# Kernel optimization log

Measured on AMD Instinct MI355X. Metric: run time of the kernel, lower is better.

## Reference

```python
import jax, jax.numpy as jnp
import numpy as np
import math

B, L, D = 8, 2048, 256
NUM_TYPES = 1
T_MAX = 200.0
SIGMA = 1.0


def setup_inputs() -> dict:
    key = jax.random.key(0)
    ks = jax.random.split(key, 12)
    event_type = jnp.ones((B, L), dtype=jnp.int64 if jax.config.jax_enable_x64 else jnp.int32)
    t = jax.random.uniform(ks[0], (B, L), dtype=jnp.float32) * T_MAX
    event_time = jnp.sort(t, axis=-1)
    s = 1.0 / math.sqrt(D)
    emb_weight = jax.random.normal(ks[1], (NUM_TYPES + 1, D), jnp.float32)
    emb_weight = emb_weight.at[0].set(0.0)  # padding_idx=0
    gate_w = jax.random.normal(ks[2], (2, D), jnp.float32) * s
    gate_b = jnp.zeros((2,), jnp.float32)
    ker_w = jax.random.normal(ks[3], (1, D), jnp.float32) * s
    ker_b = jnp.zeros((1,), jnp.float32)
    ln_gamma = jnp.ones((D,), jnp.float32)
    ln_beta = jnp.zeros((D,), jnp.float32)
    gen_input_w = jax.random.normal(ks[4], (D, D), jnp.float32) * s
    gen_noise_w = jax.random.normal(ks[5], (D, D), jnp.float32) * s
    gen_out_w = jax.random.normal(ks[6], (1, D), jnp.float32) * s
    gen_out_b = jnp.zeros((1,), jnp.float32)
    noise = jax.random.uniform(ks[7], (B, L, D), jnp.float32)  # torch.rand noise in Generator
    return dict(event_type=event_type, event_time=event_time, emb_weight=emb_weight,
                gate_w=gate_w, gate_b=gate_b, ker_w=ker_w, ker_b=ker_b,
                ln_gamma=ln_gamma, ln_beta=ln_beta, gen_input_w=gen_input_w,
                gen_noise_w=gen_noise_w, gen_out_w=gen_out_w, gen_out_b=gen_out_b,
                noise=noise)


def _softplus_beta(x, beta):
    return jax.nn.softplus(beta * x) / beta


def reference(event_type, event_time, emb_weight, gate_w, gate_b, ker_w, ker_b,
              ln_gamma, ln_beta, gen_input_w, gen_noise_w, gen_out_w, gen_out_b, noise):
    d_model = emb_weight.shape[-1]
    # ---- temporal positional encoding (this is `embedding`) ----
    pos_vec = jnp.power(10000.0, 2.0 * jnp.arange(d_model, dtype=jnp.float32) / d_model)
    t = event_time[:, :, None] / pos_vec                      # [B,L,D]
    idx = jnp.arange(d_model)
    temp_enc = jnp.where(idx % 2 == 0, jnp.sin(t), jnp.cos(t))
    # ---- type embedding ----
    te = emb_weight[event_type] * math.sqrt(d_model)          # [B,L,D]
    # ---- pairwise |t_i - t_j| ; xt[b,i,j]=t_i, xt_bar[b,i,j]=t_j ----
    dt = jnp.abs(event_time[:, :, None] - event_time[:, None, :])  # [B,L,L]
    # ---- squared exponential kernel: params depend only on row i (xd[b,i,j]=te[b,i]) ----
    ls = _softplus_beta(te @ ker_w.T + ker_b, 0.2)[..., 0]    # [B,L]
    scores_k = (SIGMA ** 2) * jnp.exp(-(dt ** 2) / (ls[:, :, None] ** 2))
    # ---- sigmoid gate ----
    p = jax.nn.sigmoid(te @ gate_w.T + gate_b)                # [B,L,2]
    l = p[..., 0][:, :, None]
    s = p[..., 1][:, :, None]
    gate = 1.0 + 0.5 * jnp.tanh((dt / T_MAX - l) / s)
    scores = scores_k * gate                                  # [B,L,L]
    # ---- causal mask: strictly-upper-triangle -> -1e10, then softmax ----
    causal = jnp.tril(jnp.ones((event_time.shape[1], event_time.shape[1]), jnp.bool_))
    scores = jnp.where(causal[None], scores, -1e10)
    attn = jax.nn.softmax(scores, axis=-1)
    # ---- hidden = attn @ temp_enc, layernorm ----
    hidden = jnp.einsum('bij,bjd->bid', attn, temp_enc)
    mu = hidden.mean(-1, keepdims=True)
    var = hidden.var(-1, keepdims=True)
    hidden = (hidden - mu) / jnp.sqrt(var + 1e-6) * ln_gamma + ln_beta
    # ---- Generator (dropout in eval = identity) ----
    h = jax.nn.relu(noise @ gen_noise_w.T + hidden @ gen_input_w.T)
    out = jax.nn.softplus(h @ gen_out_w.T + gen_out_b)[..., 0]  # [B,L]
    return out
```

## Files before the change

kernel.cpp:

```cpp
#include <hip/hip_runtime.h>
#include <hip/hip_bf16.h>

#define BD 8
#define LD 2048
#define DD 256
#define LOG2E 1.4426950408889634f

typedef unsigned short ushort_t;
typedef __attribute__((ext_vector_type(8))) short short8;
typedef __attribute__((ext_vector_type(4))) float floatx4;

__device__ __forceinline__ ushort_t f2bfu(float x) {
  __hip_bfloat16 h = __float2bfloat16(x);
  return *reinterpret_cast<ushort_t*>(&h);
}

__device__ __forceinline__ float exp2fast(float x) {
#if __has_builtin(__builtin_amdgcn_exp2f)
  return __builtin_amdgcn_exp2f(x);
#else
  return __expf(x * 0.6931471805599453f);
#endif
}

__device__ __forceinline__ void dma16(const ushort_t* g, ushort_t* l) {
  __builtin_amdgcn_global_load_lds(
      (const __attribute__((address_space(1))) unsigned int*)g,
      (__attribute__((address_space(3))) unsigned int*)l,
      16, 0, 0);
}

__device__ __forceinline__ float sin_acc(float a) {
  float k = rintf(a * 0.15915494f);
  float r = __builtin_fmaf(-k, 6.2831855f, a);
  r = __builtin_fmaf(-k, -1.7484555e-7f, r);
  return __sinf(r);
}
__device__ __forceinline__ float cos_acc(float a) {
  float k = rintf(a * 0.15915494f);
  float r = __builtin_fmaf(-k, 6.2831855f, a);
  r = __builtin_fmaf(-k, -1.7484555e-7f, r);
  return __cosf(r);
}

__device__ __forceinline__ short8 pk8(float4 a, float4 b) {
  short8 r;
  r[0] = (short)f2bfu(a.x); r[1] = (short)f2bfu(a.y);
  r[2] = (short)f2bfu(a.z); r[3] = (short)f2bfu(a.w);
  r[4] = (short)f2bfu(b.x); r[5] = (short)f2bfu(b.y);
  r[6] = (short)f2bfu(b.z); r[7] = (short)f2bfu(b.w);
  return r;
}

__global__ __launch_bounds__(256) void k_prep(
    const float* __restrict__ etime, const float* __restrict__ embw,
    const float* __restrict__ gatew, const float* __restrict__ gateb,
    const float* __restrict__ kerw, const float* __restrict__ kerb,
    const float* __restrict__ wn, const float* __restrict__ wi,
    ushort_t* __restrict__ enc_bf, ushort_t* __restrict__ wcat,
    float* __restrict__ ptable)
{
  const int bk = blockIdx.x;
  const int tid = threadIdx.x;
  __shared__ float ts[32];
  __shared__ float red[4][3];
  if (bk < 512) {
    if (tid < 32) ts[tid] = etime[(bk >> 6) * LD + (bk & 63) * 32 + tid];
    __syncthreads();
    uint4* dst = (uint4*)(enc_bf + (size_t)bk * 8192);
    #pragma unroll
    for (int jblk = 0; jblk < 4; ++jblk) {
      const int idx4 = jblk * 256 + tid;
      const int d = ((idx4 >> 6) << 4) | (idx4 & 15);
      const int jb = ((idx4 >> 4) & 3) * 8;
      float freq = __expf(-0.07195578416f * (float)d);
      unsigned int pk[4];
      #pragma unroll
      for (int p = 0; p < 4; ++p) {
        float a0 = ts[jb + 2 * p] * freq;
        float a1 = ts[jb + 2 * p + 1] * freq;
        float v0 = (d & 1) ? cos_acc(a0) : sin_acc(a0);
        float v1 = (d & 1) ? cos_acc(a1) : sin_acc(a1);
        pk[p] = (unsigned int)f2bfu(v0) | ((unsigned int)f2bfu(v1) << 16);
      }
      dst[idx4] = make_uint4(pk[0], pk[1], pk[2], pk[3]);
    }
  } else if (bk < 640) {
    int p = (bk - 512) * 256 + tid;
    int c = p >> 7;
    int k = (p & 127) * 4;
    const float* src = (k < 256) ? (wn + c * 256 + k) : (wi + c * 256 + (k - 256));
    float4 f = *(const float4*)src;
    ushort4 u;
    u.x = f2bfu(f.x); u.y = f2bfu(f.y); u.z = f2bfu(f.z); u.w = f2bfu(f.w);
    *(ushort4*)(wcat + (size_t)c * 512 + k) = u;
  } else {
    int d = tid;
    int lane = d & 63, wvi = d >> 6;
    for (int ty = 0; ty < 2; ++ty) {
      float te = embw[ty * DD + d] * 16.0f;
      float p1 = te * kerw[d];
      float p2 = te * gatew[d];
      float p3 = te * gatew[DD + d];
      #pragma unroll
      for (int off = 32; off > 0; off >>= 1) {
        p1 += __shfl_xor(p1, off);
        p2 += __shfl_xor(p2, off);
        p3 += __shfl_xor(p3, off);
      }
      if (lane == 0) { red[wvi][0] = p1; red[wvi][1] = p2; red[wvi][2] = p3; }
      __syncthreads();
      if (d == 0) {
        float s1 = red[0][0] + red[1][0] + red[2][0] + red[3][0] + kerb[0];
        float s2 = red[0][1] + red[1][1] + red[2][1] + red[3][1] + gateb[0];
        float s3 = red[0][2] + red[1][2] + red[2][2] + red[3][2] + gateb[1];
        float z = 0.2f * s1;
        float sp = (z > 15.0f) ? z : log1pf(__expf(z));
        float ls = 5.0f * sp;
        float il = 1.0f / (ls * ls);
        float l  = 1.0f / (1.0f + __expf(-s2));
        float s  = 1.0f / (1.0f + __expf(-s3));
        float is2 = 2.0f / s;
        ptable[ty * 4 + 0] = -il * LOG2E;
        ptable[ty * 4 + 1] = 0.005f * is2 * LOG2E;
        ptable[ty * 4 + 2] = l * is2 * LOG2E;
      }
      __syncthreads();
    }
  }
}

__global__ __launch_bounds__(512, 2) void k_attn(
    const ushort_t* __restrict__ enc_bf, const float* __restrict__ etime,
    const int* __restrict__ etype, const float* __restrict__ ptable,
    const float* __restrict__ gamma, const float* __restrict__ beta,
    ushort_t* __restrict__ hidden_bf)
{
  __shared__ __align__(16) ushort_t stage[8][8192];
  const int tid = threadIdx.x;
  const int lane = tid & 63, wv = tid >> 6;
  const int bk = blockIdx.x;
  const int b = bk & 7;
  const int idx = bk >> 3;
  const int myg = (wv < 4) ? (63 - idx) : idx;
  const int kwv = wv & 3;
  const int base = b * LD;
  const int m = lane & 15, kg = lane >> 4;
  const int i0 = myg * 32 + m;
  const int i1 = i0 + 16;
  const float ti0 = etime[base + i0];
  const float ti1 = etime[base + i1];
  const int ty0 = etype[base + i0] * 4;
  const int ty1 = etype[base + i1] * 4;
  const float p00 = ptable[ty0 + 0], p01 = ptable[ty0 + 1], p02 = ptable[ty0 + 2];
  const float p10 = ptable[ty1 + 0], p11 = ptable[ty1 + 1], p12 = ptable[ty1 + 2];
  floatx4 acc0[16], acc1[16];
  #pragma unroll
  for (int nt = 0; nt < 16; ++nt) {
    acc0[nt] = (floatx4){0.f, 0.f, 0.f, 0.f};
    acc1[nt] = (floatx4){0.f, 0.f, 0.f, 0.f};
  }
  const int nch = myg + 1;
  const ushort_t* __restrict__ encC = enc_bf + (size_t)(b * 64) * 8192;
  ushort_t* mybuf = &stage[wv][0];

#define WPAIR(V, MASKED)                                                      \
  {                                                                           \
    float d0 = ti0 - tj[V];                                                   \
    float d1 = ti1 - tj[V];                                                   \
    float e10 = exp2fast(d0 * d0 * p00);                                      \
    float e11 = exp2fast(d1 * d1 * p10);                                      \
    float z0 = __builtin_fmaf(fabsf(d0), p01, -p02);                          \
    float z1 = __builtin_fmaf(fabsf(d1), p11, -p12);                          \
    float r0 = __builtin_amdgcn_rcpf(exp2fast(z0) + 1.0f);                    \
    float r1 = __builtin_amdgcn_rcpf(exp2fast(z1) + 1.0f);                    \
    float w0 = exp2fast(e10 * __builtin_fmaf(r0, -LOG2E, 1.5f * LOG2E));      \
    float w1 = exp2fast(e11 * __builtin_fmaf(r1, -LOG2E, 1.5f * LOG2E));      \
    if (MASKED) {                                                             \
      w0 = (j0 + V <= i0) ? w0 : 0.0f;                                        \
      w1 = (j0 + V <= i1) ? w1 : 0.0f;                                        \
    }                                                                         \
    af0[V] = (short)f2bfu(w0);                                                \
    af1[V] = (short)f2bfu(w1);                                                \
  }

  for (int ch = kwv; ch < nch; ch += 4) {
    const int j0 = ch * 32 + kg * 8;
    float4 tja = *(const float4*)(etime + base + j0);
    float4 tjb = *(const float4*)(etime + base + j0 + 4);
    __builtin_amdgcn_s_waitcnt(0xC07F);
    const ushort_t* gsrc = encC + (size_t)ch * 8192 + lane * 8;
    #pragma unroll
    for (int nt = 0; nt < 16; ++nt)
      dma16(gsrc + nt * 512, mybuf + nt * 512);
    float tj[8] = {tja.x, tja.y, tja.z, tja.w, tjb.x, tjb.y, tjb.z, tjb.w};
    short8 af0, af1;
    if (ch < myg) {
      #pragma unroll
      for (int v = 0; v < 8; ++v) WPAIR(v, false)
    } else {
      #pragma unroll
      for (int v = 0; v < 8; ++v) WPAIR(v, true)
    }
    __builtin_amdgcn_s_waitcnt(0x0F70);
    #pragma unroll
    for (int nt = 0; nt < 16; ++nt) {
      short8 bf = *(const short8*)(mybuf + nt * 512 + lane * 8);
      acc0[nt] = __builtin_amdgcn_mfma_f32_16x16x32_bf16(af0, bf, acc0[nt], 0, 0, 0);
      acc1[nt] = __builtin_amdgcn_mfma_f32_16x16x32_bf16(af1, bf, acc1[nt], 0, 0, 0);
    }
  }
#undef WPAIR

  __syncthreads();
  floatx4* lacc = (floatx4*)&stage[0][0];
  if (wv != 0 && wv != 4) {
    const int slot = (wv < 4) ? (wv - 1) : (wv - 2);
    #pragma unroll
    for (int nt = 0; nt < 16; ++nt) lacc[(slot * 16 + nt) * 64 + lane] = acc0[nt];
  }
  __syncthreads();
  if (wv == 0 || wv == 4) {
    const int s0 = (wv == 0) ? 0 : 3;
    #pragma unroll
    for (int nt = 0; nt < 16; ++nt)
      acc0[nt] = acc0[nt] + lacc[((s0 + 0) * 16 + nt) * 64 + lane]
                          + lacc[((s0 + 1) * 16 + nt) * 64 + lane]
                          + lacc[((s0 + 2) * 16 + nt) * 64 + lane];
  }
  __syncthreads();
  if (wv != 1 && wv != 5) {
    const int slot = (wv < 4) ? ((wv == 0) ? 0 : (wv - 1)) : ((wv == 4) ? 3 : (wv - 2));
    #pragma unroll
    for (int nt = 0; nt < 16; ++nt) lacc[(slot * 16 + nt) * 64 + lane] = acc1[nt];
  }
  __syncthreads();
  if (wv == 1 || wv == 5) {
    const int s0 = (wv == 1) ? 0 : 3;
    #pragma unroll
    for (int nt = 0; nt < 16; ++nt)
      acc0[nt] = acc1[nt] + lacc[((s0 + 0) * 16 + nt) * 64 + lane]
                          + lacc[((s0 + 1) * 16 + nt) * 64 + lane]
                          + lacc[((s0 + 2) * 16 + nt) * 64 + lane];
  }
  if (wv == 0 || wv == 1 || wv == 4 || wv == 5) {
    float gl[16], cl[16];
    #pragma unroll
    for (int nt = 0; nt < 16; ++nt) { gl[nt] = gamma[nt * 16 + m]; cl[nt] = beta[nt * 16 + m]; }
    const int G = (wv < 4) ? (63 - idx) : idx;
    const int row0 = base + G * 32 + (wv & 1) * 16;
    #pragma unroll
    for (int r = 0; r < 4; ++r) {
      float h[16];
      float sm = 0.0f, sq = 0.0f;
      #pragma unroll
      for (int nt = 0; nt < 16; ++nt) {
        h[nt] = acc0[nt][r];
        sm += h[nt]; sq += h[nt] * h[nt];
      }
      #pragma unroll
      for (int off = 1; off < 16; off <<= 1) {
        sm += __shfl_xor(sm, off);
        sq += __shfl_xor(sq, off);
      }
      float mean = sm * (1.0f / 256.0f);
      float var = sq * (1.0f / 256.0f) - mean * mean;
      float rstd = rsqrtf(var + 1e-6f);
      ushort_t* dst = hidden_bf + ((size_t)(row0 + kg * 4 + r)) * DD + m;
      #pragma unroll
      for (int nt = 0; nt < 16; ++nt)
        dst[nt * 16] = f2bfu((h[nt] - mean) * rstd * gl[nt] + cl[nt]);
    }
  }
}

__global__ __launch_bounds__(256) void k_gen(
    const float* __restrict__ noise, const ushort_t* __restrict__ hidden_bf,
    const ushort_t* __restrict__ wcat, const float* __restrict__ wout,
    const float* __restrict__ bout, float* __restrict__ out)
{
  __shared__ float pbuf[4][2][16];
  const int tid = threadIdx.x;
  const int lane = tid & 63, wv = tid >> 6;
  const int m = lane & 15, kg = lane >> 4;
  const int r0 = blockIdx.x * 32 + m;
  const float* __restrict__ nf0 = noise + (size_t)r0 * DD;
  const float* __restrict__ nf1 = noise + (size_t)(r0 + 16) * DD;
  const ushort_t* __restrict__ ah0 = hidden_bf + (size_t)r0 * DD;
  const ushort_t* __restrict__ ah1 = hidden_bf + (size_t)(r0 + 16) * DD;
  floatx4 acc[2][4];
  #pragma unroll
  for (int t = 0; t < 2; ++t)
    #pragma unroll
    for (int n = 0; n < 4; ++n) acc[t][n] = (floatx4){0.f, 0.f, 0.f, 0.f};
  const ushort_t* __restrict__ bbase = wcat + ((size_t)(wv * 4) * 16 + m) * 512 + kg * 8;
  #pragma unroll
  for (int ks = 0; ks < 16; ++ks) {
    const int koff = (ks & 7) * 32 + kg * 8;
    short8 a0, a1;
    if (ks < 8) {
      float4 fa = *(const float4*)(nf0 + koff);
      float4 fb = *(const float4*)(nf0 + koff + 4);
      a0 = pk8(fa, fb);
      fa = *(const float4*)(nf1 + koff);
      fb = *(const float4*)(nf1 + koff + 4);
      a1 = pk8(fa, fb);
    } else {
      a0 = *(const short8*)(ah0 + koff);
      a1 = *(const short8*)(ah1 + koff);
    }
    const ushort_t* bp = bbase + ks * 32;
    #pragma unroll
    for (int n = 0; n < 4; ++n) {
      short8 bf = *(const short8*)(bp + (size_t)n * 8192);
      acc[0][n] = __builtin_amdgcn_mfma_f32_16x16x32_bf16(a0, bf, acc[0][n], 0, 0, 0);
      acc[1][n] = __builtin_amdgcn_mfma_f32_16x16x32_bf16(a1, bf, acc[1][n], 0, 0, 0);
    }
  }
  float wo_l[4];
  #pragma unroll
  for (int n = 0; n < 4; ++n) wo_l[n] = wout[(wv * 4 + n) * 16 + m];
  #pragma unroll
  for (int t = 0; t < 2; ++t) {
    #pragma unroll
    for (int r4 = 0; r4 < 4; ++r4) {
      float p = 0.0f;
      #pragma unroll
      for (int n = 0; n < 4; ++n) p += fmaxf(acc[t][n][r4], 0.0f) * wo_l[n];
      #pragma unroll
      for (int off = 1; off < 16; off <<= 1) p += __shfl_xor(p, off);
      if (m == 0) pbuf[wv][t][kg * 4 + r4] = p;
    }
  }
  __syncthreads();
  if (tid < 32) {
    int t = tid >> 4, rr = tid & 15;
    float x = pbuf[0][t][rr] + pbuf[1][t][rr] + pbuf[2][t][rr] + pbuf[3][t][rr] + bout[0];
    float sp = (x > 15.0f) ? x : log1pf(__expf(x));
    out[blockIdx.x * 32 + t * 16 + rr] = sp;
  }
}

extern "C" void kernel_launch(void* const* d_in, const int* in_sizes, int n_in,
                              void* d_out, int out_size, void* d_ws, size_t ws_size,
                              hipStream_t stream) {
  const int*   etype = (const int*)d_in[0];
  const float* etime = (const float*)d_in[1];
  const float* embw  = (const float*)d_in[2];
  const float* gatew = (const float*)d_in[3];
  const float* gateb = (const float*)d_in[4];
  const float* kerw  = (const float*)d_in[5];
  const float* kerb  = (const float*)d_in[6];
  const float* gamma = (const float*)d_in[7];
  const float* beta  = (const float*)d_in[8];
  const float* wi    = (const float*)d_in[9];
  const float* wn    = (const float*)d_in[10];
  const float* wo    = (const float*)d_in[11];
  const float* bo    = (const float*)d_in[12];
  const float* noise = (const float*)d_in[13];
  float* out = (float*)d_out;

  char* w8 = (char*)d_ws;
  float* ptable       = (float*)(w8);
  ushort_t* enc_bf    = (ushort_t*)(w8 + 262144);
  ushort_t* hidden_bf = (ushort_t*)(w8 + 262144 + 8388608);
  ushort_t* wcat      = (ushort_t*)(w8 + 262144 + 2 * 8388608);

  k_prep<<<641, 256, 0, stream>>>(etime, embw, gatew, gateb, kerw, kerb,
                                  wn, wi, enc_bf, wcat, ptable);
  k_attn<<<256, 512, 0, stream>>>(enc_bf, etime, etype, ptable,
                                  gamma, beta, hidden_bf);
  k_gen<<<512, 256, 0, stream>>>(noise, hidden_bf, wcat, wo, bo, out);
}
```

Before: 149.2 us.

## Share enc chunks between paired row-groups with double-buffered producer DMA

In the attention kernel, each wave used to fetch its own enc chunk into a private LDS slot. Now the four high-group waves act as producers: they double-buffer DMA of the next chunk while both row groups read the same chunk from shared LDS, with a barrier each round. This halves global enc traffic and overlaps loads with compute. Event times are also staged once in LDS. Separately, the generator kernel now runs 512-thread blocks that each cover 64 rows. The trade-off is a block-wide barrier every round, which can stall the low-group waves while they sit idle after finishing their shorter range.

```diff
diff --git a/kernel.cpp b/kernel.cpp
--- a/kernel.cpp
+++ b/kernel.cpp
@@ -137,13 +137,16 @@
     ushort_t* __restrict__ hidden_bf)
 {
   __shared__ __align__(16) ushort_t stage[8][8192];
+  __shared__ __align__(16) float tlds[2048];
   const int tid = threadIdx.x;
   const int lane = tid & 63, wv = tid >> 6;
   const int bk = blockIdx.x;
   const int b = bk & 7;
   const int idx = bk >> 3;
-  const int myg = (wv < 4) ? (63 - idx) : idx;
-  const int kwv = wv & 3;
+  const int gHI = 63 - idx;
+  const bool prod = (wv < 4);
+  const int p = wv & 3;
+  const int myg = prod ? gHI : idx;
   const int base = b * LD;
   const int m = lane & 15, kg = lane >> 4;
   const int i0 = myg * 32 + m;
@@ -154,15 +157,24 @@
   const int ty1 = etype[base + i1] * 4;
   const float p00 = ptable[ty0 + 0], p01 = ptable[ty0 + 1], p02 = ptable[ty0 + 2];
   const float p10 = ptable[ty1 + 0], p11 = ptable[ty1 + 1], p12 = ptable[ty1 + 2];
+  *(float4*)(tlds + tid * 4) = *(const float4*)(etime + base + tid * 4);
   floatx4 acc0[16], acc1[16];
   #pragma unroll
   for (int nt = 0; nt < 16; ++nt) {
     acc0[nt] = (floatx4){0.f, 0.f, 0.f, 0.f};
     acc1[nt] = (floatx4){0.f, 0.f, 0.f, 0.f};
   }
-  const int nch = myg + 1;
   const ushort_t* __restrict__ encC = enc_bf + (size_t)(b * 64) * 8192;
-  ushort_t* mybuf = &stage[wv][0];
+  __syncthreads();
+
+  if (prod) {
+    const ushort_t* gsrc = encC + (size_t)p * 8192 + lane * 8;
+    ushort_t* dstb = &stage[p][0];
+    #pragma unroll
+    for (int nt = 0; nt < 16; ++nt) dma16(gsrc + nt * 512, dstb + nt * 512);
+    __builtin_amdgcn_s_waitcnt(0x0F70);
+  }
+  __builtin_amdgcn_s_barrier();
 
 #define WPAIR(V, MASKED)                                                      \
   {                                                                           \
@@ -184,31 +196,44 @@
     af1[V] = (short)f2bfu(w1);                                                \
   }
 
-  for (int ch = kwv; ch < nch; ch += 4) {
-    const int j0 = ch * 32 + kg * 8;
-    float4 tja = *(const float4*)(etime + base + j0);
-    float4 tjb = *(const float4*)(etime + base + j0 + 4);
-    __builtin_amdgcn_s_waitcnt(0xC07F);
-    const ushort_t* gsrc = encC + (size_t)ch * 8192 + lane * 8;
-    #pragma unroll
-    for (int nt = 0; nt < 16; ++nt)
-      dma16(gsrc + nt * 512, mybuf + nt * 512);
-    float tj[8] = {tja.x, tja.y, tja.z, tja.w, tjb.x, tjb.y, tjb.z, tjb.w};
-    short8 af0, af1;
-    if (ch < myg) {
-      #pragma unroll
-      for (int v = 0; v < 8; ++v) WPAIR(v, false)
-    } else {
-      #pragma unroll
-      for (int v = 0; v < 8; ++v) WPAIR(v, true)
-    }
-    __builtin_amdgcn_s_waitcnt(0x0F70);
-    #pragma unroll
-    for (int nt = 0; nt < 16; ++nt) {
-      short8 bf = *(const short8*)(mybuf + nt * 512 + lane * 8);
-      acc0[nt] = __builtin_amdgcn_mfma_f32_16x16x32_bf16(af0, bf, acc0[nt], 0, 0, 0);
-      acc1[nt] = __builtin_amdgcn_mfma_f32_16x16x32_bf16(af1, bf, acc1[nt], 0, 0, 0);
-    }
+  const int R = (gHI >> 2) + 1;
+  for (int r = 0; r < R; ++r) {
+    const int ch = 4 * r + p;
+    if (prod) {
+      if (ch + 4 <= gHI) {
+        const ushort_t* gsrc = encC + (size_t)(ch + 4) * 8192 + lane * 8;
+        ushort_t* dstb = &stage[p + 4 * ((r + 1) & 1)][0];
+        #pragma unroll
+        for (int nt = 0; nt < 16; ++nt) dma16(gsrc + nt * 512, dstb + nt * 512);
+        __builtin_amdgcn_s_waitcnt(0x4F70);
+      } else {
+        __builtin_amdgcn_s_waitcnt(0x0F70);
+      }
+    }
+    if (ch <= myg) {
+      const int j0 = ch * 32 + kg * 8;
+      float4 tja = *(const float4*)(tlds + j0);
+      float4 tjb = *(const float4*)(tlds + j0 + 4);
+      float tj[8] = {tja.x, tja.y, tja.z, tja.w, tjb.x, tjb.y, tjb.z, tjb.w};
+      short8 af0, af1;
+      if (ch < myg) {
+        #pragma unroll
+        for (int v = 0; v < 8; ++v) WPAIR(v, false)
+      } else {
+        #pragma unroll
+        for (int v = 0; v < 8; ++v) WPAIR(v, true)
+      }
+      const ushort_t* rbuf = &stage[p + 4 * (r & 1)][0];
+      #pragma unroll
+      for (int nt = 0; nt < 16; ++nt) {
+        short8 bf = *(const short8*)(rbuf + nt * 512 + lane * 8);
+        acc0[nt] = __builtin_amdgcn_mfma_f32_16x16x32_bf16(af0, bf, acc0[nt], 0, 0, 0);
+        acc1[nt] = __builtin_amdgcn_mfma_f32_16x16x32_bf16(af1, bf, acc1[nt], 0, 0, 0);
+      }
+    }
+    asm volatile("s_waitcnt lgkmcnt(0)" ::: "memory");
+    __builtin_amdgcn_sched_barrier(0);
+    __builtin_amdgcn_s_barrier();
   }
 #undef WPAIR
 
@@ -247,7 +272,7 @@
     float gl[16], cl[16];
     #pragma unroll
     for (int nt = 0; nt < 16; ++nt) { gl[nt] = gamma[nt * 16 + m]; cl[nt] = beta[nt * 16 + m]; }
-    const int G = (wv < 4) ? (63 - idx) : idx;
+    const int G = (wv < 4) ? gHI : idx;
     const int row0 = base + G * 32 + (wv & 1) * 16;
     #pragma unroll
     for (int r = 0; r < 4; ++r) {
@@ -274,16 +299,18 @@
   }
 }
 
-__global__ __launch_bounds__(256) void k_gen(
+__global__ __launch_bounds__(512) void k_gen(
     const float* __restrict__ noise, const ushort_t* __restrict__ hidden_bf,
     const ushort_t* __restrict__ wcat, const float* __restrict__ wout,
     const float* __restrict__ bout, float* __restrict__ out)
 {
-  __shared__ float pbuf[4][2][16];
+  __shared__ float pbuf[2][4][2][16];
   const int tid = threadIdx.x;
   const int lane = tid & 63, wv = tid >> 6;
+  const int q = wv & 3;
+  const int h = wv >> 2;
   const int m = lane & 15, kg = lane >> 4;
-  const int r0 = blockIdx.x * 32 + m;
+  const int r0 = blockIdx.x * 64 + h * 32 + m;
   const float* __restrict__ nf0 = noise + (size_t)r0 * DD;
   const float* __restrict__ nf1 = noise + (size_t)(r0 + 16) * DD;
   const ushort_t* __restrict__ ah0 = hidden_bf + (size_t)r0 * DD;
@@ -293,7 +320,7 @@
   for (int t = 0; t < 2; ++t)
     #pragma unroll
     for (int n = 0; n < 4; ++n) acc[t][n] = (floatx4){0.f, 0.f, 0.f, 0.f};
-  const ushort_t* __restrict__ bbase = wcat + ((size_t)(wv * 4) * 16 + m) * 512 + kg * 8;
+  const ushort_t* __restrict__ bbase = wcat + ((size_t)(q * 4) * 16 + m) * 512 + kg * 8;
   #pragma unroll
   for (int ks = 0; ks < 16; ++ks) {
     const int koff = (ks & 7) * 32 + kg * 8;
@@ -319,7 +346,7 @@
   }
   float wo_l[4];
   #pragma unroll
-  for (int n = 0; n < 4; ++n) wo_l[n] = wout[(wv * 4 + n) * 16 + m];
+  for (int n = 0; n < 4; ++n) wo_l[n] = wout[(q * 4 + n) * 16 + m];
   #pragma unroll
   for (int t = 0; t < 2; ++t) {
     #pragma unroll
@@ -329,15 +356,16 @@
       for (int n = 0; n < 4; ++n) p += fmaxf(acc[t][n][r4], 0.0f) * wo_l[n];
       #pragma unroll
       for (int off = 1; off < 16; off <<= 1) p += __shfl_xor(p, off);
-      if (m == 0) pbuf[wv][t][kg * 4 + r4] = p;
-    }
-  }
-  __syncthreads();
-  if (tid < 32) {
-    int t = tid >> 4, rr = tid & 15;
-    float x = pbuf[0][t][rr] + pbuf[1][t][rr] + pbuf[2][t][rr] + pbuf[3][t][rr] + bout[0];
+      if (m == 0) pbuf[h][q][t][kg * 4 + r4] = p;
+    }
+  }
+  __syncthreads();
+  if (tid < 64) {
+    int h2 = tid >> 5, t = (tid >> 4) & 1, rr = tid & 15;
+    float x = pbuf[h2][0][t][rr] + pbuf[h2][1][t][rr] + pbuf[h2][2][t][rr]
+            + pbuf[h2][3][t][rr] + bout[0];
     float sp = (x > 15.0f) ? x : log1pf(__expf(x));
-    out[blockIdx.x * 32 + t * 16 + rr] = sp;
+    out[blockIdx.x * 64 + h2 * 32 + t * 16 + rr] = sp;
   }
 }
 
@@ -370,5 +398,5 @@
                                   wn, wi, enc_bf, wcat, ptable);
   k_attn<<<256, 512, 0, stream>>>(enc_bf, etime, etype, ptable,
                                   gamma, beta, hidden_bf);
-  k_gen<<<512, 256, 0, stream>>>(noise, hidden_bf, wcat, wo, bo, out);
-}
+  k_gen<<<256, 512, 0, stream>>>(noise, hidden_bf, wcat, wo, bo, out);
+}
```

After: 152.3 us. +2.1%, slower.
